# Performance work log

Measured on AMD Instinct MI355X. Metric: run time of the kernel, lower is better.

The kernel has to match this reference:

```python
import jax, jax.numpy as jnp
import numpy as np

BINS = np.array([1, 2, 3, 4, 8, 16, 32, 64], dtype=np.int32)


def setup_inputs() -> dict:
    N, G, F, H, K = 1024, 620, 20, 150, 128
    D_in = 3 * G + F  # 1880
    key = jax.random.key(0)
    ks = jax.random.split(key, 10)
    g = jax.random.normal(ks[0], (N, G), dtype=jnp.float32)
    si = jax.random.normal(ks[1], (N,), dtype=jnp.float32)
    i1 = jnp.sort(jax.random.randint(ks[2], (N,), 0, 8192)).astype(jnp.int32)
    i2 = jnp.sort(jax.random.randint(ks[3], (N,), 0, 8192)).astype(jnp.int32)
    dist_emb = jax.random.normal(ks[4], (9, F), dtype=jnp.float32) * 0.02
    W1 = jax.random.normal(ks[5], (D_in, H), dtype=jnp.float32) * (1.0 / np.sqrt(D_in))
    b1 = jnp.zeros((H,), jnp.float32)
    W2 = jax.random.normal(ks[6], (H, H), dtype=jnp.float32) * (1.0 / np.sqrt(H))
    b2 = jnp.zeros((H,), jnp.float32)
    W3 = jax.random.normal(ks[7], (H, 1), dtype=jnp.float32) * (1.0 / np.sqrt(H))
    b3 = jnp.zeros((1,), jnp.float32)
    return {"g": g, "si": si, "i1": i1, "i2": i2, "dist_emb": dist_emb,
            "W1": W1, "b1": b1, "W2": W2, "b2": b2, "W3": W3, "b3": b3, "K": K}


def reference(g, si, i1, i2, dist_emb, W1, b1, W2, b2, W3, b3, K):
    # Dropout is inference-disabled; epsilon dummy antecedent appended as last column.
    N, G = g.shape
    # span n's antecedents are spans [max(0, n-K), n); lay out as [N, K] window
    j_idx = jnp.arange(N)[:, None] - K + jnp.arange(K)[None, :]  # [N, K]
    valid = j_idx >= 0
    j = jnp.clip(j_idx, 0, N - 1)
    g_j = g[j]                      # [N, K, G] ragged gather (masked dense)
    g_i = g[:, None, :]             # [N, 1, G]
    # distance feature: bin(i.i2 - j.i1) with idx = #bins <= d
    d = i2[:, None] - i1[j]         # [N, K]
    bin_idx = jnp.searchsorted(jnp.asarray(BINS), d, side='right')
    de = dist_emb[bin_idx]          # [N, K, F]
    pairs = jnp.concatenate(
        [jnp.broadcast_to(g_i, (N, K, G)), g_j, g_i * g_j, de], axis=-1)  # [N, K, 3G+F]
    h = jax.nn.relu(jnp.einsum('nkd,dh->nkh', pairs, W1) + b1)
    h = jax.nn.relu(jnp.einsum('nkh,hm->nkm', h, W2) + b2)
    s = (jnp.einsum('nkh,ho->nko', h, W3) + b3)[..., 0]  # [N, K]
    sij = si[:, None] + si[j] + s
    sij = jnp.where(valid, sij, 0.0)
    eps = jnp.zeros((N, 1), sij.dtype)  # epsilon dummy score
    return jnp.concatenate([sij, eps], axis=-1)  # [N, K+1]
```

## Files before the change

kernel.cpp:

```cpp
#include <hip/hip_runtime.h>
#include <hip/hip_bf16.h>
#include <stdint.h>

typedef __attribute__((ext_vector_type(8))) short short8;
typedef __attribute__((ext_vector_type(4))) float float4_t;

#define N_PTS 1024
#define G_DIM 620
#define G_PAD 640
#define F_DIM 20
#define H_DIM 150
#define H_PAD 160
#define H_PAD2 192
#define K_WIN 128
#define OUT_C (K_WIN + 1)

__device__ __forceinline__ float bf2f(short u) {
  union { unsigned int i; float f; } x;
  x.i = ((unsigned int)(unsigned short)u) << 16;
  return x.f;
}
__device__ __forceinline__ short f2bf(float f) {
  union { float f; unsigned int i; } x; x.f = f;
  unsigned int u = x.i;
  u += 0x7FFFu + ((u >> 16) & 1u);
  return (short)(u >> 16);
}
__device__ __forceinline__ short f2bf_hw(float f) {
  __hip_bfloat16 h = __float2bfloat16(f);
  union { __hip_bfloat16 h; short s; } u; u.h = h;
  return u.s;
}
__device__ __forceinline__ void gload_lds16(const void* g, void* l) {
  __builtin_amdgcn_global_load_lds(
      (const __attribute__((address_space(1))) unsigned int*)g,
      (__attribute__((address_space(3))) unsigned int*)l, 16, 0, 0);
}

__global__ void prep_misc(const float* __restrict__ g, const float* __restrict__ W1,
                          const float* __restrict__ W2, const float* __restrict__ dist_emb,
                          short* __restrict__ g_bf, short* __restrict__ W1cT,
                          short* __restrict__ W2T, float* __restrict__ deW,
                          short* __restrict__ W1abT) {
  const int T1 = N_PTS * G_PAD;
  const int T2 = H_PAD * G_PAD;
  const int T3 = H_PAD * H_PAD2;
  const int T4 = 9 * H_PAD;
  const int T5 = 2 * H_PAD * G_PAD;
  const int total = T1 + T2 + T3 + T4 + T5;
  for (int t = blockIdx.x * blockDim.x + threadIdx.x; t < total;
       t += gridDim.x * blockDim.x) {
    if (t < T1) {
      int n = t / G_PAD, d = t % G_PAD;
      g_bf[t] = (d < G_DIM) ? f2bf(g[n * G_DIM + d]) : (short)0;
    } else if (t < T1 + T2) {
      int q = t - T1;
      int h = q / G_PAD, d = q % G_PAD;
      W1cT[q] = (h < H_DIM && d < G_DIM) ? f2bf(W1[(2 * G_DIM + d) * H_DIM + h]) : (short)0;
    } else if (t < T1 + T2 + T3) {
      int q = t - T1 - T2;
      int m = q / H_PAD2, k = q % H_PAD2;
      W2T[q] = (m < H_DIM && k < H_DIM) ? f2bf(W2[k * H_DIM + m]) : (short)0;
    } else if (t < T1 + T2 + T3 + T4) {
      int q = t - T1 - T2 - T3;
      int b = q / H_PAD, h = q % H_PAD;
      float acc = 0.f;
      if (h < H_DIM) {
        for (int f = 0; f < F_DIM; ++f)
          acc += dist_emb[b * F_DIM + f] * W1[(3 * G_DIM + f) * H_DIM + h];
      }
      deW[q] = acc;
    } else {
      int q = t - T1 - T2 - T3 - T4;
      int h = q / G_PAD, d = q % G_PAD;
      short v = 0;
      if (d < G_DIM) {
        if (h < H_PAD) { if (h < H_DIM) v = f2bf(W1[d * H_DIM + h]); }
        else { int col = h - H_PAD; if (col < H_DIM) v = f2bf(W1[(G_DIM + d) * H_DIM + col]); }
      }
      W1abT[q] = v;
    }
  }
}

__global__ __launch_bounds__(256) void prep_uv_mfma(
    const short* __restrict__ g_bf, const short* __restrict__ W1abT,
    const float* __restrict__ b1, float* __restrict__ U, float* __restrict__ V) {
  __shared__ __align__(16) char sA[64 * 128];
  __shared__ __align__(16) char sB[160 * 128];
  const int m0 = blockIdx.x * 64;
  const int yb = blockIdx.y * H_PAD;
  const int tid = threadIdx.x, lane = tid & 63, wid = tid >> 6;
  const int wm = wid >> 1, wn = wid & 1;
  const int lo4 = lane & 15, hi2 = lane >> 4;
  const int l8 = lane >> 3, c8 = lane & 7;
  const int xe = (c8 ^ (l8 & 7)) * 8;

  const float4_t fz = {0.f, 0.f, 0.f, 0.f};
  float4_t acc[2][5];
  #pragma unroll
  for (int a = 0; a < 2; ++a)
    #pragma unroll
    for (int b = 0; b < 5; ++b) acc[a][b] = fz;

  for (int step = 0; step < 10; ++step) {
    const int d0 = step * 64;
    #pragma unroll
    for (int cc = 0; cc < 2; ++cc) {
      int row = wid * 8 + cc * 32 + l8;
      gload_lds16(g_bf + (m0 + row) * G_PAD + d0 + xe, sA + (wid * 8 + cc * 32) * 128);
    }
    #pragma unroll
    for (int cc = 0; cc < 5; ++cc) {
      int row = wid * 8 + cc * 32 + l8;
      gload_lds16(W1abT + (yb + row) * G_PAD + d0 + xe, sB + (wid * 8 + cc * 32) * 128);
    }
    __syncthreads();
    #pragma unroll
    for (int ks = 0; ks < 2; ++ks) {
      const int kb = ks * 64 + 16 * hi2;
      short8 af[2], bq[5];
      #pragma unroll
      for (int mt = 0; mt < 2; ++mt) {
        int row = wm * 32 + mt * 16 + lo4;
        af[mt] = *((const short8*)(sA + row * 128 + (kb ^ ((row & 7) << 4))));
      }
      #pragma unroll
      for (int nt = 0; nt < 5; ++nt) {
        int row = wn * 80 + nt * 16 + lo4;
        bq[nt] = *((const short8*)(sB + row * 128 + (kb ^ ((row & 7) << 4))));
      }
      #pragma unroll
      for (int mt = 0; mt < 2; ++mt)
        #pragma unroll
        for (int nt = 0; nt < 5; ++nt)
          acc[mt][nt] = __builtin_amdgcn_mfma_f32_16x16x32_bf16(af[mt], bq[nt], acc[mt][nt], 0, 0, 0);
    }
    __syncthreads();
  }

  float* O = blockIdx.y ? V : U;
  const bool isU = (blockIdx.y == 0);
  #pragma unroll
  for (int mt = 0; mt < 2; ++mt)
    #pragma unroll
    for (int r = 0; r < 4; ++r) {
      int m = m0 + wm * 32 + mt * 16 + hi2 * 4 + r;
      #pragma unroll
      for (int nt = 0; nt < 5; ++nt) {
        int h = wn * 80 + nt * 16 + lo4;
        float v = acc[mt][nt][r];
        if (h < H_DIM) { if (isU) v += b1[h]; } else { v = 0.f; }
        O[m * H_PAD + h] = v;
      }
    }
}

__global__ __launch_bounds__(256, 2) void pair_main(
    const short* __restrict__ g_bf, const short* __restrict__ W1cT,
    const short* __restrict__ W2T, const float* __restrict__ U,
    const float* __restrict__ V, const float* __restrict__ deW,
    const float* __restrict__ si, const int* __restrict__ i1,
    const int* __restrict__ i2, const float* __restrict__ W3,
    const float* __restrict__ b2, const float* __restrict__ b3,
    float* __restrict__ out) {
  __shared__ __align__(16) char smem[73728];
  __shared__ __align__(16) short gi_s[G_PAD];
  __shared__ float sj_s[K_WIN];
  __shared__ int bin_s[K_WIN];
  __shared__ float s_buf[2][K_WIN];

  char* const P0 = smem;
  char* const P1 = smem + 16384;
  char* const B0 = smem + 32768;
  char* const B1 = smem + 53248;
  char* const Hb = smem;

  const int i = blockIdx.x;
  const int tid = threadIdx.x;
  const int lane = tid & 63;
  const int wid = tid >> 6;
  const int wm = wid >> 1, wn = wid & 1;
  const int lo4 = lane & 15, hi2 = lane >> 4;
  const int l8 = lane >> 3, c8 = lane & 7;
  const int xe = (c8 ^ (l8 & 7)) * 8;
  const int tc8 = tid & 7;

  if (tid < G_PAD / 8)
    ((short8*)gi_s)[tid] = ((const short8*)(g_bf + i * G_PAD))[tid];
  if (tid < K_WIN) {
    int jr = i - K_WIN + tid, jc = jr < 0 ? 0 : jr;
    int d = i2[i] - i1[jc];
    bin_s[tid] = (d >= 1) + (d >= 2) + (d >= 3) + (d >= 4) +
                 (d >= 8) + (d >= 16) + (d >= 32) + (d >= 64);
    sj_s[tid] = si[jc];
  }
  __syncthreads();

  auto stageB1f = [&](int step, char* B) {
    const int d0 = step * 64;
    #pragma unroll
    for (int cc = 0; cc < 5; ++cc) {
      int row = wid * 8 + cc * 32 + l8;
      gload_lds16(W1cT + row * G_PAD + d0 + xe, B + (wid * 8 + cc * 32) * 128);
    }
  };
  auto loadA = [&](int step, short8* gjv, short8& gvv) {
    const int d0 = step * 64;
    gvv = *((const short8*)(gi_s + d0 + tc8 * 8));
    #pragma unroll
    for (int cc = 0; cc < 4; ++cc) {
      int c = tid + 256 * cc, row = c >> 3;
      int jr = i - K_WIN + row, jc = jr < 0 ? 0 : jr;
      gjv[cc] = *((const short8*)(g_bf + jc * G_PAD + d0 + tc8 * 8));
    }
  };
  auto writeP = [&](char* P, const short8* gjv, const short8& gvv) {
    #pragma unroll
    for (int cc = 0; cc < 4; ++cc) {
      int c = tid + 256 * cc, row = c >> 3;
      short8 p;
      #pragma unroll
      for (int e = 0; e < 8; ++e) p[e] = f2bf_hw(bf2f(gjv[cc][e]) * bf2f(gvv[e]));
      int byte = row * 128 + ((tc8 * 16) ^ ((row & 7) << 4));
      *((short8*)(P + byte)) = p;
    }
  };

  {
    short8 gjv[4], gvv;
    stageB1f(0, B0);
    loadA(0, gjv, gvv);
    writeP(P0, gjv, gvv);
  }

  const float4_t fz = {0.f, 0.f, 0.f, 0.f};
  float4_t acc[4][5];
  #pragma unroll
  for (int a = 0; a < 4; ++a)
    #pragma unroll
    for (int b = 0; b < 5; ++b) acc[a][b] = fz;

  for (int step = 0; step < 10; ++step) {
    char* Pc = (step & 1) ? P1 : P0;
    char* Bc = (step & 1) ? B1 : B0;
    char* Pn = (step & 1) ? P0 : P1;
    char* Bn = (step & 1) ? B0 : B1;
    __syncthreads();
    short8 gjv[4], gvv;
    if (step < 9) {
      stageB1f(step + 1, Bn);
      loadA(step + 1, gjv, gvv);
    }
    #pragma unroll
    for (int ks = 0; ks < 2; ++ks) {
      const int kb = ks * 64 + 16 * hi2;
      short8 af[4], bq[5];
      #pragma unroll
      for (int mt = 0; mt < 4; ++mt) {
        int row = wm * 64 + mt * 16 + lo4;
        af[mt] = *((const short8*)(Pc + row * 128 + (kb ^ ((row & 7) << 4))));
      }
      #pragma unroll
      for (int nt = 0; nt < 5; ++nt) {
        int row = wn * 80 + nt * 16 + lo4;
        bq[nt] = *((const short8*)(Bc + row * 128 + (kb ^ ((row & 7) << 4))));
      }
      #pragma unroll
      for (int mt = 0; mt < 4; ++mt)
        #pragma unroll
        for (int nt = 0; nt < 5; ++nt)
          acc[mt][nt] = __builtin_amdgcn_mfma_f32_16x16x32_bf16(af[mt], bq[nt], acc[mt][nt], 0, 0, 0);
    }
    if (step < 9) writeP(Pn, gjv, gvv);
  }
  __syncthreads();

  const float* Ui = U + i * H_PAD;
  #pragma unroll
  for (int mt = 0; mt < 4; ++mt) {
    #pragma unroll
    for (int r = 0; r < 4; ++r) {
      int m = wm * 64 + mt * 16 + hi2 * 4 + r;
      int jr = i - K_WIN + m, jc = jr < 0 ? 0 : jr;
      const float* Vj = V + jc * H_PAD;
      const float* De = deW + bin_s[m] * H_PAD;
      #pragma unroll
      for (int nt = 0; nt < 5; ++nt) {
        int h = wn * 80 + nt * 16 + lo4;
        float val = acc[mt][nt][r] + Ui[h] + Vj[h] + De[h];
        val = (h < H_DIM) ? fmaxf(val, 0.f) : 0.f;
        int tile = h >> 6, hc = h & 63;
        int byte = tile * 16384 + m * 128 + ((hc * 2) ^ ((m & 7) << 4));
        *((short*)(Hb + byte)) = f2bf_hw(val);
      }
    }
  }

  float4_t acc2[4][5];
  #pragma unroll
  for (int a = 0; a < 4; ++a)
    #pragma unroll
    for (int b = 0; b < 5; ++b) acc2[a][b] = fz;

  #pragma unroll
  for (int t2 = 0; t2 < 3; ++t2) {
    #pragma unroll
    for (int cc = 0; cc < 5; ++cc) {
      int row = wid * 8 + cc * 32 + l8;
      gload_lds16(W2T + row * H_PAD2 + t2 * 64 + xe, B1 + (wid * 8 + cc * 32) * 128);
    }
    __syncthreads();
    #pragma unroll
    for (int ks = 0; ks < 2; ++ks) {
      if (t2 == 2 && ks == 1) continue;
      const int kb = ks * 64 + 16 * hi2;
      short8 af[4], bq[5];
      #pragma unroll
      for (int mt = 0; mt < 4; ++mt) {
        int row = wm * 64 + mt * 16 + lo4;
        af[mt] = *((const short8*)(Hb + t2 * 16384 + row * 128 + (kb ^ ((row & 7) << 4))));
      }
      #pragma unroll
      for (int nt = 0; nt < 5; ++nt) {
        int row = wn * 80 + nt * 16 + lo4;
        bq[nt] = *((const short8*)(B1 + row * 128 + (kb ^ ((row & 7) << 4))));
      }
      #pragma unroll
      for (int mt = 0; mt < 4; ++mt)
        #pragma unroll
        for (int nt = 0; nt < 5; ++nt)
          acc2[mt][nt] = __builtin_amdgcn_mfma_f32_16x16x32_bf16(af[mt], bq[nt], acc2[mt][nt], 0, 0, 0);
    }
    __syncthreads();
  }

  float sp[4][4];
  #pragma unroll
  for (int mt = 0; mt < 4; ++mt)
    #pragma unroll
    for (int r = 0; r < 4; ++r) sp[mt][r] = 0.f;

  #pragma unroll
  for (int nt = 0; nt < 5; ++nt) {
    int h = wn * 80 + nt * 16 + lo4;
    float w3 = (h < H_DIM) ? W3[h] : 0.f;
    float bb = (h < H_DIM) ? b2[h] : 0.f;
    #pragma unroll
    for (int mt = 0; mt < 4; ++mt)
      #pragma unroll
      for (int r = 0; r < 4; ++r) {
        float hv = fmaxf(acc2[mt][nt][r] + bb, 0.f);
        sp[mt][r] += hv * w3;
      }
  }
  #pragma unroll
  for (int mt = 0; mt < 4; ++mt)
    #pragma unroll
    for (int r = 0; r < 4; ++r) {
      float v = sp[mt][r];
      v += __shfl_xor(v, 1);
      v += __shfl_xor(v, 2);
      v += __shfl_xor(v, 4);
      v += __shfl_xor(v, 8);
      sp[mt][r] = v;
    }
  if (lo4 == 0) {
    #pragma unroll
    for (int mt = 0; mt < 4; ++mt)
      #pragma unroll
      for (int r = 0; r < 4; ++r) {
        int m = wm * 64 + mt * 16 + hi2 * 4 + r;
        s_buf[wn][m] = sp[mt][r];
      }
  }
  __syncthreads();

  if (tid < K_WIN) {
    int m = tid;
    int jr = i - K_WIN + m;
    float sij = si[i] + sj_s[m] + s_buf[0][m] + s_buf[1][m] + b3[0];
    out[i * OUT_C + m] = (jr >= 0) ? sij : 0.f;
  }
  if (tid == K_WIN) out[i * OUT_C + K_WIN] = 0.f;
}

extern "C" void kernel_launch(void* const* d_in, const int* in_sizes, int n_in,
                              void* d_out, int out_size, void* d_ws, size_t ws_size,
                              hipStream_t stream) {
  const float* g  = (const float*)d_in[0];
  const float* si = (const float*)d_in[1];
  const int*   i1 = (const int*)d_in[2];
  const int*   i2 = (const int*)d_in[3];
  const float* de = (const float*)d_in[4];
  const float* W1 = (const float*)d_in[5];
  const float* b1 = (const float*)d_in[6];
  const float* W2 = (const float*)d_in[7];
  const float* b2 = (const float*)d_in[8];
  const float* W3 = (const float*)d_in[9];
  const float* b3 = (const float*)d_in[10];
  float* out = (float*)d_out;

  char* ws = (char*)d_ws;
  short* g_bf  = (short*)(ws);
  short* W1cT  = (short*)(ws + 1310720);
  short* W2T   = (short*)(ws + 1515520);
  float* U     = (float*)(ws + 1576960);
  float* V     = (float*)(ws + 2232320);
  float* deW   = (float*)(ws + 2887680);
  short* W1abT = (short*)(ws + 2893440);

  prep_misc<<<1024, 256, 0, stream>>>(g, W1, W2, de, g_bf, W1cT, W2T, deW, W1abT);
  prep_uv_mfma<<<dim3(16, 2), 256, 0, stream>>>(g_bf, W1abT, b1, U, V);
  pair_main<<<N_PTS, 256, 0, stream>>>(g_bf, W1cT, W2T, U, V, deW, si, i1, i2, W3, b2, b3, out);
}
```

Before: 80.26 us.

## Restructure pair kernel with BK=32 register pipeline, folded bias/dist GEMM, tiled prep

Rewrites the prep kernel into role-partitioned blocks with an LDS-tiled W1 transpose and vectorized g conversion. The pair kernel now uses a K-step of 32 with padded LDS rows instead of swizzled rows, and register-staged loads in place of global_load_lds. It folds the U bias and the distance embedding into an extra MFMA step using one-hot A rows. The W2 GEMM reads B directly from global memory into registers. It also shrinks LDS so three blocks can share a CU, and remaps block ids for L2 locality. The risks are more pipeline steps and more syncs, plus some loss of precision from storing U in bf16.

```diff
diff --git a/kernel.cpp b/kernel.cpp
--- a/kernel.cpp
+++ b/kernel.cpp
@@ -11,9 +11,11 @@
 #define F_DIM 20
 #define H_DIM 150
 #define H_PAD 160
-#define H_PAD2 192
 #define K_WIN 128
 #define OUT_C (K_WIN + 1)
+#define BK 32
+#define NSTEP 20
+#define PSTR 80
 
 __device__ __forceinline__ float bf2f(short u) {
   union { unsigned int i; float f; } x;
@@ -37,55 +39,91 @@
       (__attribute__((address_space(3))) unsigned int*)l, 16, 0, 0);
 }
 
-__global__ void prep_misc(const float* __restrict__ g, const float* __restrict__ W1,
+__global__ void prep_pack(const float* __restrict__ g, const float* __restrict__ W1,
                           const float* __restrict__ W2, const float* __restrict__ dist_emb,
                           short* __restrict__ g_bf, short* __restrict__ W1cT,
-                          short* __restrict__ W2T, float* __restrict__ deW,
-                          short* __restrict__ W1abT) {
-  const int T1 = N_PTS * G_PAD;
-  const int T2 = H_PAD * G_PAD;
-  const int T3 = H_PAD * H_PAD2;
-  const int T4 = 9 * H_PAD;
-  const int T5 = 2 * H_PAD * G_PAD;
-  const int total = T1 + T2 + T3 + T4 + T5;
-  for (int t = blockIdx.x * blockDim.x + threadIdx.x; t < total;
-       t += gridDim.x * blockDim.x) {
-    if (t < T1) {
-      int n = t / G_PAD, d = t % G_PAD;
-      g_bf[t] = (d < G_DIM) ? f2bf(g[n * G_DIM + d]) : (short)0;
-    } else if (t < T1 + T2) {
-      int q = t - T1;
-      int h = q / G_PAD, d = q % G_PAD;
-      W1cT[q] = (h < H_DIM && d < G_DIM) ? f2bf(W1[(2 * G_DIM + d) * H_DIM + h]) : (short)0;
-    } else if (t < T1 + T2 + T3) {
-      int q = t - T1 - T2;
-      int m = q / H_PAD2, k = q % H_PAD2;
+                          short* __restrict__ W1abT, short* __restrict__ W2T,
+                          short* __restrict__ deWT) {
+  __shared__ float lds[32 * 165];
+  __shared__ float dw[9 * H_PAD];
+  const int bx = blockIdx.x, tid = threadIdx.x;
+  if (bx < 256) {
+    const int n0 = bx * 4;
+    for (int c = tid; c < 320; c += 256) {
+      int r = c / 80, cc = c - r * 80;
+      int n = n0 + r, d0 = cc * 8;
+      short8 o;
+      if (d0 + 8 <= G_DIM) {
+        const float* src = g + n * G_DIM + d0;
+        #pragma unroll
+        for (int e = 0; e < 8; ++e) o[e] = f2bf(src[e]);
+      } else {
+        #pragma unroll
+        for (int e = 0; e < 8; ++e) {
+          int d = d0 + e;
+          o[e] = (d < G_DIM) ? f2bf(g[n * G_DIM + d]) : (short)0;
+        }
+      }
+      *(short8*)(g_bf + n * G_PAD + d0) = o;
+    }
+  } else if (bx < 316) {
+    const int tb = bx - 256;
+    const int third = tb / 20, dt = tb - third * 20;
+    const int d0 = dt * 32;
+    for (int c = tid; c < 1280; c += 256) {
+      int dr = c / 40, ch4 = c - dr * 40;
+      int dd = d0 + dr;
+      int w1r = third * G_DIM + dd;
+      #pragma unroll
+      for (int e = 0; e < 4; ++e) {
+        int h = ch4 * 4 + e;
+        lds[dr * 165 + h] = (dd < G_DIM && h < H_DIM) ? W1[w1r * H_DIM + h] : 0.f;
+      }
+    }
+    __syncthreads();
+    short* outp = (third == 2) ? W1cT : (W1abT + third * H_PAD * G_PAD);
+    for (int c = tid; c < 640; c += 256) {
+      int h = c >> 2, ch = c & 3;
+      short8 o;
+      #pragma unroll
+      for (int e = 0; e < 8; ++e) o[e] = f2bf(lds[(ch * 8 + e) * 165 + h]);
+      *(short8*)(outp + h * G_PAD + d0 + ch * 8) = o;
+    }
+  } else if (bx < 320) {
+    const int base = (bx - 316) * 6400;
+    for (int c = tid; c < 6400; c += 256) {
+      int q = base + c;
+      int m = q / H_PAD, k = q - m * H_PAD;
       W2T[q] = (m < H_DIM && k < H_DIM) ? f2bf(W2[k * H_DIM + m]) : (short)0;
-    } else if (t < T1 + T2 + T3 + T4) {
-      int q = t - T1 - T2 - T3;
-      int b = q / H_PAD, h = q % H_PAD;
+    }
+  } else {
+    for (int c = tid; c < 9 * H_PAD; c += 256) {
+      int b = c / H_PAD, h = c - b * H_PAD;
       float acc = 0.f;
-      if (h < H_DIM) {
+      if (h < H_DIM)
         for (int f = 0; f < F_DIM; ++f)
           acc += dist_emb[b * F_DIM + f] * W1[(3 * G_DIM + f) * H_DIM + h];
-      }
-      deW[q] = acc;
-    } else {
-      int q = t - T1 - T2 - T3 - T4;
-      int h = q / G_PAD, d = q % G_PAD;
-      short v = 0;
-      if (d < G_DIM) {
-        if (h < H_PAD) { if (h < H_DIM) v = f2bf(W1[d * H_DIM + h]); }
-        else { int col = h - H_PAD; if (col < H_DIM) v = f2bf(W1[(G_DIM + d) * H_DIM + col]); }
-      }
-      W1abT[q] = v;
+      dw[c] = acc;
+    }
+    __syncthreads();
+    if (tid < H_PAD) {
+      #pragma unroll
+      for (int ch = 0; ch < 4; ++ch) {
+        short8 o;
+        #pragma unroll
+        for (int e = 0; e < 8; ++e) {
+          int kk = ch * 8 + e;
+          o[e] = (kk < 9) ? f2bf(dw[kk * H_PAD + tid]) : (short)0;
+        }
+        *(short8*)(deWT + tid * 32 + ch * 8) = o;
+      }
     }
   }
 }
 
 __global__ __launch_bounds__(256) void prep_uv_mfma(
     const short* __restrict__ g_bf, const short* __restrict__ W1abT,
-    const float* __restrict__ b1, float* __restrict__ U, float* __restrict__ V) {
+    const float* __restrict__ b1, short* __restrict__ U_bf, float* __restrict__ V) {
   __shared__ __align__(16) char sA[64 * 128];
   __shared__ __align__(16) char sB[160 * 128];
   const int m0 = blockIdx.x * 64;
@@ -139,7 +177,6 @@
     __syncthreads();
   }
 
-  float* O = blockIdx.y ? V : U;
   const bool isU = (blockIdx.y == 0);
   #pragma unroll
   for (int mt = 0; mt < 2; ++mt)
@@ -150,41 +187,45 @@
       for (int nt = 0; nt < 5; ++nt) {
         int h = wn * 80 + nt * 16 + lo4;
         float v = acc[mt][nt][r];
-        if (h < H_DIM) { if (isU) v += b1[h]; } else { v = 0.f; }
-        O[m * H_PAD + h] = v;
-      }
-    }
-}
-
-__global__ __launch_bounds__(256, 2) void pair_main(
+        if (isU) {
+          v = (h < H_DIM) ? v + b1[h] : 0.f;
+          U_bf[m * H_PAD + h] = f2bf(v);
+        } else {
+          V[m * H_PAD + h] = (h < H_DIM) ? v : 0.f;
+        }
+      }
+    }
+}
+
+__global__ __launch_bounds__(256, 3) void pair_main(
     const short* __restrict__ g_bf, const short* __restrict__ W1cT,
-    const short* __restrict__ W2T, const float* __restrict__ U,
-    const float* __restrict__ V, const float* __restrict__ deW,
+    const short* __restrict__ W2T, const short* __restrict__ U_bf,
+    const float* __restrict__ V, const short* __restrict__ deWT,
     const float* __restrict__ si, const int* __restrict__ i1,
     const int* __restrict__ i2, const float* __restrict__ W3,
     const float* __restrict__ b2, const float* __restrict__ b3,
     float* __restrict__ out) {
-  __shared__ __align__(16) char smem[73728];
+  __shared__ __align__(16) char smem[49152];
   __shared__ __align__(16) short gi_s[G_PAD];
   __shared__ float sj_s[K_WIN];
   __shared__ int bin_s[K_WIN];
   __shared__ float s_buf[2][K_WIN];
 
   char* const P0 = smem;
-  char* const P1 = smem + 16384;
-  char* const B0 = smem + 32768;
-  char* const B1 = smem + 53248;
+  char* const P1 = smem + 10240;
+  char* const B0 = smem + 20480;
+  char* const B1 = smem + 33280;
   char* const Hb = smem;
 
-  const int i = blockIdx.x;
+  const int bid = blockIdx.x;
+  const int i = ((bid & 7) << 7) | (bid >> 3);
   const int tid = threadIdx.x;
   const int lane = tid & 63;
   const int wid = tid >> 6;
   const int wm = wid >> 1, wn = wid & 1;
   const int lo4 = lane & 15, hi2 = lane >> 4;
-  const int l8 = lane >> 3, c8 = lane & 7;
-  const int xe = (c8 ^ (l8 & 7)) * 8;
-  const int tc8 = tid & 7;
+  const int rA = tid >> 2;
+  const int cA = tid & 3;
 
   if (tid < G_PAD / 8)
     ((short8*)gi_s)[tid] = ((const short8*)(g_bf + i * G_PAD))[tid];
@@ -197,42 +238,51 @@
   }
   __syncthreads();
 
-  auto stageB1f = [&](int step, char* B) {
-    const int d0 = step * 64;
-    #pragma unroll
-    for (int cc = 0; cc < 5; ++cc) {
-      int row = wid * 8 + cc * 32 + l8;
-      gload_lds16(W1cT + row * G_PAD + d0 + xe, B + (wid * 8 + cc * 32) * 128);
+  int jr0 = i - K_WIN + rA;        int jc0 = jr0 < 0 ? 0 : jr0;
+  int jr1 = i - K_WIN + rA + 64;   int jc1 = jr1 < 0 ? 0 : jr1;
+  const short* gpA0 = g_bf + jc0 * G_PAD + cA * 8;
+  const short* gpA1 = g_bf + jc1 * G_PAD + cA * 8;
+  const short* wb0 = W1cT + rA * G_PAD + cA * 8;
+  const short* wb1 = W1cT + (rA + 64) * G_PAD + cA * 8;
+  const short* wb2 = W1cT + (rA + 128) * G_PAD + cA * 8;
+
+  short8 ra0, ra1, rgv, rb0, rb1, rb2;
+  auto issue_loads = [&](int s) {
+    if (s < NSTEP) {
+      const int d0 = s * BK;
+      rgv = *(const short8*)(gi_s + d0 + cA * 8);
+      ra0 = *(const short8*)(gpA0 + d0);
+      ra1 = *(const short8*)(gpA1 + d0);
+      rb0 = *(const short8*)(wb0 + d0);
+      rb1 = *(const short8*)(wb1 + d0);
+      if (tid < 128) rb2 = *(const short8*)(wb2 + d0);
+    } else {
+      int bv0 = bin_s[rA], bv1 = bin_s[rA + 64];
+      #pragma unroll
+      for (int e = 0; e < 8; ++e) {
+        int kk = cA * 8 + e;
+        ra0[e] = (kk == bv0 || kk == 9) ? (short)0x3F80 : (short)0;
+        ra1[e] = (kk == bv1 || kk == 9) ? (short)0x3F80 : (short)0;
+        rgv[e] = (short)0x3F80;
+      }
+      rb0 = *(const short8*)(deWT + rA * BK + cA * 8);
+      rb1 = *(const short8*)(deWT + (rA + 64) * BK + cA * 8);
+      if (tid < 128) rb2 = *(const short8*)(deWT + (rA + 128) * BK + cA * 8);
     }
   };
-  auto loadA = [&](int step, short8* gjv, short8& gvv) {
-    const int d0 = step * 64;
-    gvv = *((const short8*)(gi_s + d0 + tc8 * 8));
-    #pragma unroll
-    for (int cc = 0; cc < 4; ++cc) {
-      int c = tid + 256 * cc, row = c >> 3;
-      int jr = i - K_WIN + row, jc = jr < 0 ? 0 : jr;
-      gjv[cc] = *((const short8*)(g_bf + jc * G_PAD + d0 + tc8 * 8));
-    }
+  auto write_stage = [&](char* P, char* B) {
+    short8 p0, p1;
+    #pragma unroll
+    for (int e = 0; e < 8; ++e) {
+      p0[e] = f2bf_hw(bf2f(ra0[e]) * bf2f(rgv[e]));
+      p1[e] = f2bf_hw(bf2f(ra1[e]) * bf2f(rgv[e]));
+    }
+    *(short8*)(P + rA * PSTR + cA * 16) = p0;
+    *(short8*)(P + (rA + 64) * PSTR + cA * 16) = p1;
+    *(short8*)(B + rA * PSTR + cA * 16) = rb0;
+    *(short8*)(B + (rA + 64) * PSTR + cA * 16) = rb1;
+    if (tid < 128) *(short8*)(B + (rA + 128) * PSTR + cA * 16) = rb2;
   };
-  auto writeP = [&](char* P, const short8* gjv, const short8& gvv) {
-    #pragma unroll
-    for (int cc = 0; cc < 4; ++cc) {
-      int c = tid + 256 * cc, row = c >> 3;
-      short8 p;
-      #pragma unroll
-      for (int e = 0; e < 8; ++e) p[e] = f2bf_hw(bf2f(gjv[cc][e]) * bf2f(gvv[e]));
-      int byte = row * 128 + ((tc8 * 16) ^ ((row & 7) << 4));
-      *((short8*)(P + byte)) = p;
-    }
-  };
-
-  {
-    short8 gjv[4], gvv;
-    stageB1f(0, B0);
-    loadA(0, gjv, gvv);
-    writeP(P0, gjv, gvv);
-  }
 
   const float4_t fz = {0.f, 0.f, 0.f, 0.f};
   float4_t acc[4][5];
@@ -241,30 +291,31 @@
     #pragma unroll
     for (int b = 0; b < 5; ++b) acc[a][b] = fz;
 
-  for (int step = 0; step < 10; ++step) {
-    char* Pc = (step & 1) ? P1 : P0;
-    char* Bc = (step & 1) ? B1 : B0;
-    char* Pn = (step & 1) ? P0 : P1;
-    char* Bn = (step & 1) ? B0 : B1;
+  issue_loads(0);
+  write_stage(P0, B0);
+
+  for (int s = 0; s <= NSTEP; ++s) {
+    char* Pc = (s & 1) ? P1 : P0;
+    char* Bc = (s & 1) ? B1 : B0;
+    char* Pn = (s & 1) ? P0 : P1;
+    char* Bn = (s & 1) ? B0 : B1;
     __syncthreads();
-    short8 gjv[4], gvv;
-    if (step < 9) {
-      stageB1f(step + 1, Bn);
-      loadA(step + 1, gjv, gvv);
-    }
-    #pragma unroll
-    for (int ks = 0; ks < 2; ++ks) {
-      const int kb = ks * 64 + 16 * hi2;
+    if (s == NSTEP) {
+      if (tid < H_PAD) *(short*)(Bc + tid * PSTR + 18) = U_bf[i * H_PAD + tid];
+      __syncthreads();
+    }
+    if (s < NSTEP) issue_loads(s + 1);
+    {
       short8 af[4], bq[5];
       #pragma unroll
       for (int mt = 0; mt < 4; ++mt) {
         int row = wm * 64 + mt * 16 + lo4;
-        af[mt] = *((const short8*)(Pc + row * 128 + (kb ^ ((row & 7) << 4))));
+        af[mt] = *((const short8*)(Pc + row * PSTR + hi2 * 16));
       }
       #pragma unroll
       for (int nt = 0; nt < 5; ++nt) {
         int row = wn * 80 + nt * 16 + lo4;
-        bq[nt] = *((const short8*)(Bc + row * 128 + (kb ^ ((row & 7) << 4))));
+        bq[nt] = *((const short8*)(Bc + row * PSTR + hi2 * 16));
       }
       #pragma unroll
       for (int mt = 0; mt < 4; ++mt)
@@ -272,11 +323,10 @@
         for (int nt = 0; nt < 5; ++nt)
           acc[mt][nt] = __builtin_amdgcn_mfma_f32_16x16x32_bf16(af[mt], bq[nt], acc[mt][nt], 0, 0, 0);
     }
-    if (step < 9) writeP(Pn, gjv, gvv);
+    if (s < NSTEP) write_stage(Pn, Bn);
   }
   __syncthreads();
 
-  const float* Ui = U + i * H_PAD;
   #pragma unroll
   for (int mt = 0; mt < 4; ++mt) {
     #pragma unroll
@@ -284,11 +334,10 @@
       int m = wm * 64 + mt * 16 + hi2 * 4 + r;
       int jr = i - K_WIN + m, jc = jr < 0 ? 0 : jr;
       const float* Vj = V + jc * H_PAD;
-      const float* De = deW + bin_s[m] * H_PAD;
       #pragma unroll
       for (int nt = 0; nt < 5; ++nt) {
         int h = wn * 80 + nt * 16 + lo4;
-        float val = acc[mt][nt][r] + Ui[h] + Vj[h] + De[h];
+        float val = acc[mt][nt][r] + Vj[h];
         val = (h < H_DIM) ? fmaxf(val, 0.f) : 0.f;
         int tile = h >> 6, hc = h & 63;
         int byte = tile * 16384 + m * 128 + ((hc * 2) ^ ((m & 7) << 4));
@@ -296,6 +345,15 @@
       }
     }
   }
+  {
+    short8 z = {0, 0, 0, 0, 0, 0, 0, 0};
+    for (int c = tid; c < 512; c += 256) {
+      int row = c >> 2, cb = c & 3;
+      int byte = 2 * 16384 + row * 128 + ((64 + cb * 16) ^ ((row & 7) << 4));
+      *((short8*)(Hb + byte)) = z;
+    }
+  }
+  __syncthreads();
 
   float4_t acc2[4][5];
   #pragma unroll
@@ -303,36 +361,34 @@
     #pragma unroll
     for (int b = 0; b < 5; ++b) acc2[a][b] = fz;
 
-  #pragma unroll
-  for (int t2 = 0; t2 < 3; ++t2) {
-    #pragma unroll
-    for (int cc = 0; cc < 5; ++cc) {
-      int row = wid * 8 + cc * 32 + l8;
-      gload_lds16(W2T + row * H_PAD2 + t2 * 64 + xe, B1 + (wid * 8 + cc * 32) * 128);
-    }
-    __syncthreads();
-    #pragma unroll
-    for (int ks = 0; ks < 2; ++ks) {
-      if (t2 == 2 && ks == 1) continue;
-      const int kb = ks * 64 + 16 * hi2;
-      short8 af[4], bq[5];
-      #pragma unroll
-      for (int mt = 0; mt < 4; ++mt) {
-        int row = wm * 64 + mt * 16 + lo4;
-        af[mt] = *((const short8*)(Hb + t2 * 16384 + row * 128 + (kb ^ ((row & 7) << 4))));
-      }
+  short8 bql[2][5];
+  #pragma unroll
+  for (int nt = 0; nt < 5; ++nt) {
+    int row = wn * 80 + nt * 16 + lo4;
+    bql[0][nt] = *(const short8*)(W2T + row * H_PAD + hi2 * 8);
+  }
+  #pragma unroll
+  for (int ks = 0; ks < 5; ++ks) {
+    const int cur = ks & 1;
+    if (ks < 4) {
       #pragma unroll
       for (int nt = 0; nt < 5; ++nt) {
         int row = wn * 80 + nt * 16 + lo4;
-        bq[nt] = *((const short8*)(B1 + row * 128 + (kb ^ ((row & 7) << 4))));
-      }
-      #pragma unroll
-      for (int mt = 0; mt < 4; ++mt)
-        #pragma unroll
-        for (int nt = 0; nt < 5; ++nt)
-          acc2[mt][nt] = __builtin_amdgcn_mfma_f32_16x16x32_bf16(af[mt], bq[nt], acc2[mt][nt], 0, 0, 0);
-    }
-    __syncthreads();
+        bql[cur ^ 1][nt] = *(const short8*)(W2T + row * H_PAD + (ks + 1) * BK + hi2 * 8);
+      }
+    }
+    short8 af[4];
+    #pragma unroll
+    for (int mt = 0; mt < 4; ++mt) {
+      int row = wm * 64 + mt * 16 + lo4;
+      int kb = (ks & 1) * 64 + hi2 * 16;
+      af[mt] = *((const short8*)(Hb + (ks >> 1) * 16384 + row * 128 + (kb ^ ((row & 7) << 4))));
+    }
+    #pragma unroll
+    for (int mt = 0; mt < 4; ++mt)
+      #pragma unroll
+      for (int nt = 0; nt < 5; ++nt)
+        acc2[mt][nt] = __builtin_amdgcn_mfma_f32_16x16x32_bf16(af[mt], bql[cur][nt], acc2[mt][nt], 0, 0, 0);
   }
 
   float sp[4][4];
@@ -404,13 +460,14 @@
   char* ws = (char*)d_ws;
   short* g_bf  = (short*)(ws);
   short* W1cT  = (short*)(ws + 1310720);
-  short* W2T   = (short*)(ws + 1515520);
-  float* U     = (float*)(ws + 1576960);
-  float* V     = (float*)(ws + 2232320);
-  float* deW   = (float*)(ws + 2887680);
-  short* W1abT = (short*)(ws + 2893440);
-
-  prep_misc<<<1024, 256, 0, stream>>>(g, W1, W2, de, g_bf, W1cT, W2T, deW, W1abT);
-  prep_uv_mfma<<<dim3(16, 2), 256, 0, stream>>>(g_bf, W1abT, b1, U, V);
-  pair_main<<<N_PTS, 256, 0, stream>>>(g_bf, W1cT, W2T, U, V, deW, si, i1, i2, W3, b2, b3, out);
-}
+  short* W1abT = (short*)(ws + 1515520);
+  short* W2T   = (short*)(ws + 1925120);
+  float* V     = (float*)(ws + 1976320);
+  short* U_bf  = (short*)(ws + 2631680);
+  short* deWT  = (short*)(ws + 2959360);
+
+  prep_pack<<<321, 256, 0, stream>>>(g, W1, W2, de, g_bf, W1cT, W1abT, W2T, deWT);
+  prep_uv_mfma<<<dim3(16, 2), 256, 0, stream>>>(g_bf, W1abT, b1, U_bf, V);
+  pair_main<<<N_PTS, 256, 0, stream>>>(g_bf, W1cT, W2T, U_bf, V, deWT,
+                                       si, i1, i2, W3, b2, b3, out);
+}
```

New measurement: 80.53 us. No clear change (+0.3%).
